# Kernel tuning notes

Measured on AMD Instinct MI355X. Metric: run time of the kernel, lower is better.

## Reference

```python
import jax, jax.numpy as jnp
import numpy as np

D_MODEL = 2048
N_HEADS = 16
HEAD_DIM = D_MODEL // N_HEADS  # 128
B, T = 2, 2048


def setup_inputs() -> dict:
    key = jax.random.key(0)
    ks = jax.random.split(key, 9)
    s = 0.02
    x = jax.random.normal(ks[0], (B, T, D_MODEL), dtype=jnp.float32)
    # Per-head projection weights (stacked over heads); torch Linear y = x @ W^T + b,
    # here W is stored as [H, d_model, head_dim] so y = einsum('btc,hcd->bhtd').
    Wq = jax.random.normal(ks[1], (N_HEADS, D_MODEL, HEAD_DIM), dtype=jnp.float32) * s
    bq = jax.random.normal(ks[2], (N_HEADS, HEAD_DIM), dtype=jnp.float32) * s
    Wk = jax.random.normal(ks[3], (N_HEADS, D_MODEL, HEAD_DIM), dtype=jnp.float32) * s
    bk = jax.random.normal(ks[4], (N_HEADS, HEAD_DIM), dtype=jnp.float32) * s
    Wv = jax.random.normal(ks[5], (N_HEADS, D_MODEL, HEAD_DIM), dtype=jnp.float32) * s
    bv = jax.random.normal(ks[6], (N_HEADS, HEAD_DIM), dtype=jnp.float32) * s
    Wo = jax.random.normal(ks[7], (D_MODEL, D_MODEL), dtype=jnp.float32) * s  # used as y @ Wo
    bo = jax.random.normal(ks[8], (D_MODEL,), dtype=jnp.float32) * s
    return {"x": x, "Wq": Wq, "bq": bq, "Wk": Wk, "bk": bk,
            "Wv": Wv, "bv": bv, "Wo": Wo, "bo": bo}


def reference(x, Wq, bq, Wk, bk, Wv, bv, Wo, bo):
    # x: [B, T, C]; per-head Q/K/V projections -> [B, H, T, D]
    Bn, Tn, C = x.shape
    H, _, D = Wq.shape
    scale = D ** (-0.5)
    q = jnp.einsum('btc,hcd->bhtd', x, Wq) + bq[None, :, None, :]
    k = jnp.einsum('btc,hcd->bhtd', x, Wk) + bk[None, :, None, :]
    v = jnp.einsum('btc,hcd->bhtd', x, Wv) + bv[None, :, None, :]
    # scores [B, H, T, T] with additive causal mask (finfo.min above the diagonal)
    scores = jnp.einsum('bhtd,bhsd->bhts', q, k) * scale
    neg = jnp.finfo(scores.dtype).min
    causal = jnp.triu(jnp.full((Tn, Tn), neg, dtype=scores.dtype), k=1)
    probs = jax.nn.softmax(scores + causal, axis=-1)
    y = jnp.einsum('bhts,bhsd->bhtd', probs, v)  # [B, H, T, D]
    # concat heads along feature dim (head order preserved) then output projection
    y = y.transpose(0, 2, 1, 3).reshape(Bn, Tn, H * D)
    return y @ Wo + bo
```

## Files before the change

kernel.cpp:

```cpp
#include <hip/hip_runtime.h>
#include <stdint.h>

typedef unsigned short u16;
typedef __attribute__((ext_vector_type(4))) u16 u16x4;
typedef __attribute__((ext_vector_type(8))) u16 u16x8;
typedef __attribute__((ext_vector_type(8))) __bf16 bf16x8;
typedef __attribute__((ext_vector_type(4))) float f32x4;

#define D_MODEL 2048
#define N_HEADS 16
#define HEAD_DIM 128
#define BATCH 2
#define SEQ 2048
#define M_TOT (BATCH*SEQ)
#define N_QKV (3*D_MODEL)

__device__ __forceinline__ u16 f2b(float f) {
  union { float f; uint32_t u; } c; c.f = f;
  uint32_t u = c.u;
  uint32_t r = (u + 0x7fffu + ((u >> 16) & 1u)) >> 16;
  return (u16)r;
}

__device__ __forceinline__ void gl_lds16(const u16* g, u16* l) {
  __builtin_amdgcn_global_load_lds(
      (const __attribute__((address_space(1))) uint32_t*)g,
      (__attribute__((address_space(3))) uint32_t*)l, 16, 0, 0);
}


__global__ void cast_x_kernel(const float* __restrict__ x, u16* __restrict__ xb, int n) {
  int i = (blockIdx.x * blockDim.x + threadIdx.x) * 4;
  if (i >= n) return;
  f32x4 v = *(const f32x4*)(x + i);
  u16x4 o;
  o[0] = f2b(v[0]); o[1] = f2b(v[1]); o[2] = f2b(v[2]); o[3] = f2b(v[3]);
  *(u16x4*)(xb + i) = o;
}

__global__ void trans_wqkv_kernel(const float* __restrict__ Wq, const float* __restrict__ Wk,
                                  const float* __restrict__ Wv, u16* __restrict__ Wt) {
  __shared__ u16 Tl[128][72];
  const int hh = blockIdx.y;
  const int qkv = hh >> 4, h = hh & 15;
  const float* src = (qkv == 0 ? Wq : qkv == 1 ? Wk : Wv) + (size_t)h * 2048 * 128;
  const int k0 = blockIdx.x * 64;
  const int tid = threadIdx.x;
  for (int it = 0; it < 32; ++it) {
    int idx = it * 256 + tid;
    int k = idx >> 7, d = idx & 127;
    Tl[d][k] = f2b(src[(size_t)(k0 + k) * 128 + d]);
  }
  __syncthreads();
  for (int it = 0; it < 32; ++it) {
    int idx = it * 256 + tid;
    int d = idx >> 6, kk = idx & 63;
    Wt[(size_t)(hh * 128 + d) * 2048 + k0 + kk] = Tl[d][kk];
  }
}

__global__ void trans_wo_kernel(const float* __restrict__ Wo, u16* __restrict__ Wot) {
  __shared__ u16 Tl[128][72];
  const int k0 = blockIdx.x * 64;
  const int n0 = blockIdx.y * 128;
  const int tid = threadIdx.x;
  for (int it = 0; it < 32; ++it) {
    int idx = it * 256 + tid;
    int k = idx >> 7, n = idx & 127;
    Tl[n][k] = f2b(Wo[(size_t)(k0 + k) * 2048 + n0 + n]);
  }
  __syncthreads();
  for (int it = 0; it < 32; ++it) {
    int idx = it * 256 + tid;
    int d = idx >> 6, kk = idx & 63;
    Wot[(size_t)(n0 + d) * 2048 + k0 + kk] = Tl[d][kk];
  }
}

__global__ void transpose_v_kernel(const u16* __restrict__ vb, u16* __restrict__ vt) {
  __shared__ u16 Tl[128 * 65];
  const int bh = blockIdx.y;
  const int t0 = blockIdx.x * 64;
  const int tid = threadIdx.x;
  const u16* src = vb + (size_t)bh * 2048 * 128;
  u16* dstp = vt + (size_t)bh * 128 * 2048;
#pragma unroll
  for (int c = 0; c < 4; ++c) {
    int ci = c * 256 + tid;
    int tr = ci >> 4, d0 = (ci & 15) * 8;
    u16x8 v = *(const u16x8*)(src + (size_t)(t0 + tr) * 128 + d0);
#pragma unroll
    for (int e = 0; e < 8; ++e) Tl[(d0 + e) * 65 + tr] = v[e];
  }
  __syncthreads();
#pragma unroll
  for (int it = 0; it < 32; ++it) {
    int idx = it * 256 + tid;
    int d = idx >> 6, tt = idx & 63;
    dstp[(size_t)d * 2048 + t0 + ((tt & 15) * 4 + (tt >> 4))] = Tl[d * 65 + tt];
  }
}

template <int EPI>
__global__ __launch_bounds__(256) void gemm_kernel(
    const u16* __restrict__ A, const u16* __restrict__ B,
    u16* __restrict__ qo, u16* __restrict__ ko, u16* __restrict__ vo,
    const float* __restrict__ bq, const float* __restrict__ bk, const float* __restrict__ bv,
    float* __restrict__ outf, const float* __restrict__ bo) {
  __shared__ u16 As[128 * 32];
  __shared__ u16 Bs[128 * 32];
  constexpr int NX = (EPI == 0) ? 48 : 16;
  const int nwg = gridDim.x;
  const int q8 = nwg >> 3;
  const int bid0 = blockIdx.x;
  const int gid = (bid0 & 7) * q8 + (bid0 >> 3);
  const int m0 = (gid / NX) * 128, n0 = (gid % NX) * 128;

  const int tid = threadIdx.x;
  const int lane = tid & 63, wv = tid >> 6;
  const int wm = (wv >> 1) * 64, wn = (wv & 1) * 64;
  const int lr = lane & 15, lk = (lane >> 4) * 8;

  f32x4 zero = {0.f, 0.f, 0.f, 0.f};
  f32x4 acc[4][4];
#pragma unroll
  for (int i = 0; i < 4; ++i)
#pragma unroll
    for (int j = 0; j < 4; ++j) acc[i][j] = zero;

  const int e0 = tid * 8;
  const int row0 = e0 >> 5;
  const int col0 = e0 & 31;
  const u16* Ag = A + (size_t)(m0 + row0) * 2048 + col0;
  const u16* Bg = B + (size_t)(n0 + row0) * 2048 + col0;

  for (int kt = 0; kt < 2048; kt += 32) {
    gl_lds16(Ag + kt, As + e0);
    gl_lds16(Ag + kt + (size_t)64 * 2048, As + e0 + 64 * 32);
    gl_lds16(Bg + kt, Bs + e0);
    gl_lds16(Bg + kt + (size_t)64 * 2048, Bs + e0 + 64 * 32);
    __syncthreads();
    bf16x8 af[4], bfm[4];
#pragma unroll
    for (int i = 0; i < 4; ++i) af[i] = *(const bf16x8*)(As + (wm + i * 16 + lr) * 32 + lk);
#pragma unroll
    for (int j = 0; j < 4; ++j) bfm[j] = *(const bf16x8*)(Bs + (wn + j * 16 + lr) * 32 + lk);
#pragma unroll
    for (int i = 0; i < 4; ++i)
#pragma unroll
      for (int j = 0; j < 4; ++j)
        acc[i][j] = __builtin_amdgcn_mfma_f32_16x16x32_bf16(af[i], bfm[j], acc[i][j], 0, 0, 0);
    __syncthreads();
  }

  const int rbase = (lane >> 4) * 4;
  if (EPI == 0) {
    const int qkv = n0 >> 11, h = (n0 >> 7) & 15;
    const float* bias = (qkv == 0) ? bq : (qkv == 1) ? bk : bv;
    u16* dst = (qkv == 0) ? qo : (qkv == 1) ? ko : vo;
    const float qscale = 0.08838834764831845f * 1.4426950408889634f;
#pragma unroll
    for (int i = 0; i < 4; ++i)
#pragma unroll
      for (int j = 0; j < 4; ++j)
#pragma unroll
        for (int r = 0; r < 4; ++r) {
          int gm = m0 + wm + i * 16 + rbase + r;
          int d = wn + j * 16 + (lane & 15);
          float val = acc[i][j][r] + bias[h * 128 + d];
          if (qkv == 0) val *= qscale;
          int b = gm >> 11, t = gm & 2047;
          dst[((size_t)(b * 16 + h) * 2048 + t) * 128 + d] = f2b(val);
        }
  } else {
#pragma unroll
    for (int i = 0; i < 4; ++i)
#pragma unroll
      for (int j = 0; j < 4; ++j)
#pragma unroll
        for (int r = 0; r < 4; ++r) {
          int gm = m0 + wm + i * 16 + rbase + r;
          int gn = n0 + wn + j * 16 + (lane & 15);
          outf[(size_t)gm * 2048 + gn] = acc[i][j][r] + bo[gn];
        }
  }
}

__global__ __launch_bounds__(256) void attn_kernel(
    const u16* __restrict__ qg, const u16* __restrict__ kg,
    const u16* __restrict__ vtg, u16* __restrict__ y) {
  __shared__ u16 Kb[2][64 * 128];
  __shared__ u16 Vb[2][128 * 64];
  __shared__ u16 Pl[4][32 * 64];
  const int tid = threadIdx.x, lane = tid & 63, w = tid >> 6;
  const int bid = blockIdx.x;
  const int bh = bid & 31, qt = 15 - (bid >> 5);
  const int b = bh >> 4, h = bh & 15;
  const int lr = lane & 15, lk = (lane >> 4) * 8;
  const u16* Qp = qg + (size_t)bh * (2048 * 128);
  const u16* Kp = kg + (size_t)bh * (2048 * 128);
  const u16* Vp = vtg + (size_t)bh * (128 * 2048);

  int koff[4], voff[4], dstc[4];
#pragma unroll
  for (int c = 0; c < 4; ++c) {
    int ci = c * 256 + tid;
    dstc[c] = ci * 8;
    int kr = ci >> 4, kj = ci & 15;
    koff[c] = kr * 128 + (kj ^ (kr & 7)) * 8;
    int vd = ci >> 3, vj = ci & 7;
    voff[c] = vd * 2048 + (vj ^ (vd & 7)) * 8;
  }
  const int kxor = (lr & 7) << 4;
  const int rbase = (lane >> 4) * 4;
  const f32x4 zero = {0.f, 0.f, 0.f, 0.f};

  const int q0 = qt * 128;
  const int qw = q0 + w * 32;
  const int nt = 2 * qt + 2;

  bf16x8 qf[2][4];
#pragma unroll
  for (int s = 0; s < 2; ++s)
#pragma unroll
    for (int i = 0; i < 4; ++i)
      qf[s][i] = *(const bf16x8*)(Qp + (size_t)(qw + s * 16 + lr) * 128 + i * 32 + lk);

  f32x4 o[2][8];
#pragma unroll
  for (int s = 0; s < 2; ++s)
#pragma unroll
    for (int f = 0; f < 8; ++f) o[s][f] = zero;
  float mrow[2][4], lrow[2][4];
#pragma unroll
  for (int s = 0; s < 2; ++s)
#pragma unroll
    for (int r = 0; r < 4; ++r) { mrow[s][r] = -1e30f; lrow[s][r] = 0.f; }

#pragma unroll
  for (int c = 0; c < 4; ++c) gl_lds16(Kp + koff[c], Kb[0] + dstc[c]);
#pragma unroll
  for (int c = 0; c < 4; ++c) gl_lds16(Vp + voff[c], Vb[0] + dstc[c]);
  __syncthreads();

  int cur = 0;
  for (int t = 0; t < nt; ++t) {
    const int s0 = t * 64;
    if (t + 1 < nt) {
      const size_t skn = (size_t)(s0 + 64) * 128;
#pragma unroll
      for (int c = 0; c < 4; ++c) gl_lds16(Kp + skn + koff[c], Kb[cur ^ 1] + dstc[c]);
#pragma unroll
      for (int c = 0; c < 4; ++c) gl_lds16(Vp + (s0 + 64) + voff[c], Vb[cur ^ 1] + dstc[c]);
    }
    if (s0 <= qw + 31) {
      const char* Kc = (const char*)Kb[cur];
      f32x4 sf[2][4];
      __builtin_amdgcn_s_setprio(1);
#pragma unroll
      for (int sj = 0; sj < 4; ++sj) {
        f32x4 a0 = zero, a1 = zero;
#pragma unroll
        for (int i = 0; i < 4; ++i) {
          bf16x8 kf = *(const bf16x8*)(Kc + ((((sj * 16 + lr) * 256) + (i * 32 + lk) * 2) ^ kxor));
          a0 = __builtin_amdgcn_mfma_f32_16x16x32_bf16(qf[0][i], kf, a0, 0, 0, 0);
          a1 = __builtin_amdgcn_mfma_f32_16x16x32_bf16(qf[1][i], kf, a1, 0, 0, 0);
        }
        sf[0][sj] = a0; sf[1][sj] = a1;
      }
      __builtin_amdgcn_s_setprio(0);

      char* Pc = (char*)Pl[w];
      const bool diag = (s0 + 63 > qw);
      float pmax[2][4];
      bool need = false;
#pragma unroll
      for (int s = 0; s < 2; ++s)
#pragma unroll
        for (int r = 0; r < 4; ++r) {
          if (diag) {
            const int rq = qw + s * 16 + rbase + r;
#pragma unroll
            for (int sj = 0; sj < 4; ++sj)
              if (s0 + sj * 16 + lr > rq) sf[s][sj][r] = -1e30f;
          }
          float pm = fmaxf(fmaxf(sf[s][0][r], sf[s][1][r]),
                           fmaxf(sf[s][2][r], sf[s][3][r]));
          pmax[s][r] = pm;
          need |= (pm > mrow[s][r] + 8.f);
        }
      if (__any(need)) {
#pragma unroll
        for (int s = 0; s < 2; ++s)
#pragma unroll
          for (int r = 0; r < 4; ++r) {
            float pm = pmax[s][r];
            pm = fmaxf(pm, __shfl_xor(pm, 1));
            pm = fmaxf(pm, __shfl_xor(pm, 2));
            pm = fmaxf(pm, __shfl_xor(pm, 4));
            pm = fmaxf(pm, __shfl_xor(pm, 8));
            float mnew = fmaxf(mrow[s][r], pm);
            float sfac = __builtin_amdgcn_exp2f(mrow[s][r] - mnew);
            mrow[s][r] = mnew;
            lrow[s][r] *= sfac;
#pragma unroll
            for (int f = 0; f < 8; ++f) o[s][f][r] *= sfac;
          }
      }
#pragma unroll
      for (int s = 0; s < 2; ++s)
#pragma unroll
        for (int r = 0; r < 4; ++r) {
          const int prow = s * 16 + rbase + r;
          u16x4 pk;
          float ps = 0.f;
#pragma unroll
          for (int sj = 0; sj < 4; ++sj) {
            float p = __builtin_amdgcn_exp2f(sf[s][sj][r] - mrow[s][r]);
            ps += p;
            pk[sj] = f2b(p);
          }
          lrow[s][r] += ps;
          *(u16x4*)(Pc + ((prow * 128 + lr * 8) ^ ((prow & 7) << 4))) = pk;
        }

      const char* Vc = (const char*)Vb[cur];
      __builtin_amdgcn_s_setprio(1);
#pragma unroll
      for (int st = 0; st < 2; ++st) {
        bf16x8 pf0 = *(const bf16x8*)(Pc + (((lr * 128) + (st * 32 + lk) * 2) ^ kxor));
        bf16x8 pf1 = *(const bf16x8*)(Pc + ((((16 + lr) * 128) + (st * 32 + lk) * 2) ^ kxor));
#pragma unroll
        for (int f = 0; f < 8; ++f) {
          bf16x8 vf = *(const bf16x8*)(Vc + ((((f * 16 + lr) * 128) + (st * 32 + lk) * 2) ^ kxor));
          o[0][f] = __builtin_amdgcn_mfma_f32_16x16x32_bf16(pf0, vf, o[0][f], 0, 0, 0);
          o[1][f] = __builtin_amdgcn_mfma_f32_16x16x32_bf16(pf1, vf, o[1][f], 0, 0, 0);
        }
      }
      __builtin_amdgcn_s_setprio(0);
    }
    __syncthreads();
    cur ^= 1;
  }

#pragma unroll
  for (int s = 0; s < 2; ++s)
#pragma unroll
    for (int r = 0; r < 4; ++r) {
      float l = lrow[s][r];
      l += __shfl_xor(l, 1);
      l += __shfl_xor(l, 2);
      l += __shfl_xor(l, 4);
      l += __shfl_xor(l, 8);
      const float rinv = __builtin_amdgcn_rcpf(l);
      const int row = qw + s * 16 + rbase + r;
#pragma unroll
      for (int f = 0; f < 8; ++f)
        y[((size_t)b * 2048 + row) * 2048 + h * 128 + f * 16 + lr] =
            f2b(o[s][f][r] * rinv);
    }
}


extern "C" void kernel_launch(void* const* d_in, const int* in_sizes, int n_in,
                              void* d_out, int out_size, void* d_ws, size_t ws_size,
                              hipStream_t stream) {
  const float* x  = (const float*)d_in[0];
  const float* Wq = (const float*)d_in[1];
  const float* bq = (const float*)d_in[2];
  const float* Wk = (const float*)d_in[3];
  const float* bk = (const float*)d_in[4];
  const float* Wv = (const float*)d_in[5];
  const float* bv = (const float*)d_in[6];
  const float* Wo = (const float*)d_in[7];
  const float* bo = (const float*)d_in[8];
  float* out = (float*)d_out;
  char* ws = (char*)d_ws;

  u16* xb  = (u16*)(ws + 0);
  u16* Wt  = (u16*)(ws + 16777216);
  u16* qb  = (u16*)(ws + 41943040);
  u16* kb  = (u16*)(ws + 58720256);
  u16* vb  = (u16*)(ws + 75497472);
  u16* Wot = Wt;
  u16* vtb = (u16*)(ws + 25165824);
  u16* yb  = xb;

  cast_x_kernel<<<8192, 256, 0, stream>>>(x, xb, M_TOT * D_MODEL);
  trans_wqkv_kernel<<<dim3(32, 48), 256, 0, stream>>>(Wq, Wk, Wv, Wt);
  gemm_kernel<0><<<N_QKV / 128 * (M_TOT / 128), 256, 0, stream>>>(
      xb, Wt, qb, kb, vb, bq, bk, bv, nullptr, nullptr);
  trans_wo_kernel<<<dim3(32, 16), 256, 0, stream>>>(Wo, Wot);
  transpose_v_kernel<<<dim3(32, 32), 256, 0, stream>>>(vb, vtb);
  attn_kernel<<<512, 256, 0, stream>>>(qb, kb, vtb, yb);
  gemm_kernel<1><<<D_MODEL / 128 * (M_TOT / 128), 256, 0, stream>>>(
      yb, Wot, nullptr, nullptr, nullptr, nullptr, nullptr, nullptr, out, bo);
}
```

Baseline: 306.5 us.

## Rewrite GEMMs as 256x128 tiles with triple-buffered swizzled LDS pipeline

```diff
diff --git a/kernel.cpp b/kernel.cpp
--- a/kernel.cpp
+++ b/kernel.cpp
@@ -102,55 +102,119 @@
 }
 
 template <int EPI>
-__global__ __launch_bounds__(256) void gemm_kernel(
+__global__ __launch_bounds__(512, 2) void gemm256_kernel(
     const u16* __restrict__ A, const u16* __restrict__ B,
     u16* __restrict__ qo, u16* __restrict__ ko, u16* __restrict__ vo,
     const float* __restrict__ bq, const float* __restrict__ bk, const float* __restrict__ bv,
     float* __restrict__ outf, const float* __restrict__ bo) {
-  __shared__ u16 As[128 * 32];
-  __shared__ u16 Bs[128 * 32];
+  __shared__ u16 As[3][256 * 64];
+  __shared__ u16 Bs[3][128 * 64];
   constexpr int NX = (EPI == 0) ? 48 : 16;
-  const int nwg = gridDim.x;
-  const int q8 = nwg >> 3;
-  const int bid0 = blockIdx.x;
+  const int nwg = gridDim.x, q8 = nwg >> 3, bid0 = blockIdx.x;
   const int gid = (bid0 & 7) * q8 + (bid0 >> 3);
-  const int m0 = (gid / NX) * 128, n0 = (gid % NX) * 128;
+  const int m0 = (gid / NX) * 256, n0 = (gid % NX) * 128;
 
   const int tid = threadIdx.x;
-  const int lane = tid & 63, wv = tid >> 6;
-  const int wm = (wv >> 1) * 64, wn = (wv & 1) * 64;
+  const int lane = tid & 63, w = tid >> 6;
+  const int wm = (w >> 2) * 128, wn = (w & 3) * 32;
   const int lr = lane & 15, lk = (lane >> 4) * 8;
 
-  f32x4 zero = {0.f, 0.f, 0.f, 0.f};
-  f32x4 acc[4][4];
-#pragma unroll
-  for (int i = 0; i < 4; ++i)
-#pragma unroll
-    for (int j = 0; j < 4; ++j) acc[i][j] = zero;
-
-  const int e0 = tid * 8;
-  const int row0 = e0 >> 5;
-  const int col0 = e0 & 31;
-  const u16* Ag = A + (size_t)(m0 + row0) * 2048 + col0;
-  const u16* Bg = B + (size_t)(n0 + row0) * 2048 + col0;
-
-  for (int kt = 0; kt < 2048; kt += 32) {
-    gl_lds16(Ag + kt, As + e0);
-    gl_lds16(Ag + kt + (size_t)64 * 2048, As + e0 + 64 * 32);
-    gl_lds16(Bg + kt, Bs + e0);
-    gl_lds16(Bg + kt + (size_t)64 * 2048, Bs + e0 + 64 * 32);
-    __syncthreads();
-    bf16x8 af[4], bfm[4];
-#pragma unroll
-    for (int i = 0; i < 4; ++i) af[i] = *(const bf16x8*)(As + (wm + i * 16 + lr) * 32 + lk);
-#pragma unroll
-    for (int j = 0; j < 4; ++j) bfm[j] = *(const bf16x8*)(Bs + (wn + j * 16 + lr) * 32 + lk);
+  int aoff[4], adst[4], boff[2], bdst[2];
+#pragma unroll
+  for (int l = 0; l < 4; ++l) {
+    int ci = l * 512 + tid, row = ci >> 3, j = ci & 7;
+    aoff[l] = (m0 + row) * 2048 + (j ^ (row & 7)) * 8;
+    adst[l] = ci * 8;
+  }
+#pragma unroll
+  for (int l = 0; l < 2; ++l) {
+    int ci = l * 512 + tid, row = ci >> 3, j = ci & 7;
+    boff[l] = (n0 + row) * 2048 + (j ^ (row & 7)) * 8;
+    bdst[l] = ci * 8;
+  }
+
+  f32x4 acc[8][2];
+  const f32x4 zero = {0.f, 0.f, 0.f, 0.f};
+#pragma unroll
+  for (int i = 0; i < 8; ++i) { acc[i][0] = zero; acc[i][1] = zero; }
+
+#pragma unroll
+  for (int s = 0; s < 2; ++s) {
+#pragma unroll
+    for (int l = 0; l < 4; ++l) gl_lds16(A + aoff[l] + s * 64, As[s] + adst[l]);
+#pragma unroll
+    for (int l = 0; l < 2; ++l) gl_lds16(B + boff[l] + s * 64, Bs[s] + bdst[l]);
+  }
+  asm volatile("s_waitcnt vmcnt(6)" ::: "memory");
+  __builtin_amdgcn_s_barrier();
+
+  int slot = 0;
+  for (int kt = 0; kt < 32; ++kt) {
+    const char* Ac = (const char*)As[slot];
+    const char* Bc = (const char*)Bs[slot];
+    const int s2 = (slot + 2 >= 3) ? slot - 1 : slot + 2;
+    const bool st = (kt < 30);
+    const int k2 = (kt + 2) * 64;
+
+    bf16x8 af[4][2], bfr[2][2];
+#pragma unroll
+    for (int i = 0; i < 4; ++i) {
+      const int row = wm + i * 16 + lr;
+      const int rb = row * 128, rx = (row & 7) << 4;
+#pragma unroll
+      for (int kk = 0; kk < 2; ++kk)
+        af[i][kk] = *(const bf16x8*)(Ac + ((rb + (kk * 32 + lk) * 2) ^ rx));
+    }
+#pragma unroll
+    for (int j = 0; j < 2; ++j) {
+      const int row = wn + j * 16 + lr;
+      const int rb = row * 128, rx = (row & 7) << 4;
+#pragma unroll
+      for (int kk = 0; kk < 2; ++kk)
+        bfr[j][kk] = *(const bf16x8*)(Bc + ((rb + (kk * 32 + lk) * 2) ^ rx));
+    }
+    if (st) {
+      gl_lds16(A + aoff[0] + k2, As[s2] + adst[0]);
+      gl_lds16(A + aoff[1] + k2, As[s2] + adst[1]);
+      gl_lds16(B + boff[0] + k2, Bs[s2] + bdst[0]);
+    }
+    __builtin_amdgcn_s_setprio(1);
 #pragma unroll
     for (int i = 0; i < 4; ++i)
 #pragma unroll
-      for (int j = 0; j < 4; ++j)
-        acc[i][j] = __builtin_amdgcn_mfma_f32_16x16x32_bf16(af[i], bfm[j], acc[i][j], 0, 0, 0);
-    __syncthreads();
+      for (int j = 0; j < 2; ++j)
+#pragma unroll
+        for (int kk = 0; kk < 2; ++kk)
+          acc[i][j] = __builtin_amdgcn_mfma_f32_16x16x32_bf16(af[i][kk], bfr[j][kk], acc[i][j], 0, 0, 0);
+    __builtin_amdgcn_s_setprio(0);
+    __builtin_amdgcn_s_barrier();
+
+#pragma unroll
+    for (int i = 0; i < 4; ++i) {
+      const int row = wm + 64 + i * 16 + lr;
+      const int rb = row * 128, rx = (row & 7) << 4;
+#pragma unroll
+      for (int kk = 0; kk < 2; ++kk)
+        af[i][kk] = *(const bf16x8*)(Ac + ((rb + (kk * 32 + lk) * 2) ^ rx));
+    }
+    if (st) {
+      gl_lds16(A + aoff[2] + k2, As[s2] + adst[2]);
+      gl_lds16(A + aoff[3] + k2, As[s2] + adst[3]);
+      gl_lds16(B + boff[1] + k2, Bs[s2] + bdst[1]);
+    }
+    __builtin_amdgcn_s_setprio(1);
+#pragma unroll
+    for (int i = 0; i < 4; ++i)
+#pragma unroll
+      for (int j = 0; j < 2; ++j)
+#pragma unroll
+        for (int kk = 0; kk < 2; ++kk)
+          acc[i + 4][j] = __builtin_amdgcn_mfma_f32_16x16x32_bf16(af[i][kk], bfr[j][kk], acc[i + 4][j], 0, 0, 0);
+    __builtin_amdgcn_s_setprio(0);
+    if (kt == 30)      asm volatile("s_waitcnt vmcnt(0)" ::: "memory");
+    else if (kt < 30)  asm volatile("s_waitcnt vmcnt(6)" ::: "memory");
+    __builtin_amdgcn_s_barrier();
+    slot = (slot + 1 >= 3) ? 0 : slot + 1;
   }
 
   const int rbase = (lane >> 4) * 4;
@@ -160,13 +224,13 @@
     u16* dst = (qkv == 0) ? qo : (qkv == 1) ? ko : vo;
     const float qscale = 0.08838834764831845f * 1.4426950408889634f;
 #pragma unroll
-    for (int i = 0; i < 4; ++i)
-#pragma unroll
-      for (int j = 0; j < 4; ++j)
+    for (int i = 0; i < 8; ++i)
+#pragma unroll
+      for (int j = 0; j < 2; ++j)
 #pragma unroll
         for (int r = 0; r < 4; ++r) {
           int gm = m0 + wm + i * 16 + rbase + r;
-          int d = wn + j * 16 + (lane & 15);
+          int d = wn + j * 16 + lr;
           float val = acc[i][j][r] + bias[h * 128 + d];
           if (qkv == 0) val *= qscale;
           int b = gm >> 11, t = gm & 2047;
@@ -174,13 +238,13 @@
         }
   } else {
 #pragma unroll
-    for (int i = 0; i < 4; ++i)
-#pragma unroll
-      for (int j = 0; j < 4; ++j)
+    for (int i = 0; i < 8; ++i)
+#pragma unroll
+      for (int j = 0; j < 2; ++j)
 #pragma unroll
         for (int r = 0; r < 4; ++r) {
           int gm = m0 + wm + i * 16 + rbase + r;
-          int gn = n0 + wn + j * 16 + (lane & 15);
+          int gn = n0 + wn + j * 16 + lr;
           outf[(size_t)gm * 2048 + gn] = acc[i][j][r] + bo[gn];
         }
   }
@@ -388,11 +452,11 @@
 
   cast_x_kernel<<<8192, 256, 0, stream>>>(x, xb, M_TOT * D_MODEL);
   trans_wqkv_kernel<<<dim3(32, 48), 256, 0, stream>>>(Wq, Wk, Wv, Wt);
-  gemm_kernel<0><<<N_QKV / 128 * (M_TOT / 128), 256, 0, stream>>>(
+  gemm256_kernel<0><<<768, 512, 0, stream>>>(
       xb, Wt, qb, kb, vb, bq, bk, bv, nullptr, nullptr);
   trans_wo_kernel<<<dim3(32, 16), 256, 0, stream>>>(Wo, Wot);
   transpose_v_kernel<<<dim3(32, 32), 256, 0, stream>>>(vb, vtb);
   attn_kernel<<<512, 256, 0, stream>>>(qb, kb, vtb, yb);
-  gemm_kernel<1><<<D_MODEL / 128 * (M_TOT / 128), 256, 0, stream>>>(
+  gemm256_kernel<1><<<256, 512, 0, stream>>>(
       yb, Wot, nullptr, nullptr, nullptr, nullptr, nullptr, nullptr, out, bo);
 }
```

Result: faster. 287.8 us (-6.1%).

## Rewrite GEMMs with 256-wide tiles, 4-stage LDS pipeline and swizzled layout

Applied to the files above, without the earlier changes.

```diff
diff --git a/kernel.cpp b/kernel.cpp
--- a/kernel.cpp
+++ b/kernel.cpp
@@ -26,6 +26,14 @@
   __builtin_amdgcn_global_load_lds(
       (const __attribute__((address_space(1))) uint32_t*)g,
       (__attribute__((address_space(3))) uint32_t*)l, 16, 0, 0);
+}
+
+template <int N> __device__ __forceinline__ void waitvm() {
+  if constexpr (N == 8)      asm volatile("s_waitcnt vmcnt(8)" ::: "memory");
+  else if constexpr (N == 6) asm volatile("s_waitcnt vmcnt(6)" ::: "memory");
+  else if constexpr (N == 4) asm volatile("s_waitcnt vmcnt(4)" ::: "memory");
+  else if constexpr (N == 3) asm volatile("s_waitcnt vmcnt(3)" ::: "memory");
+  else                       asm volatile("s_waitcnt vmcnt(0)" ::: "memory");
 }
 
 
@@ -101,86 +109,135 @@
   }
 }
 
-template <int EPI>
-__global__ __launch_bounds__(256) void gemm_kernel(
+template <int EPI, int BM>
+__global__ __launch_bounds__(512, 2) void gemm256_kernel(
     const u16* __restrict__ A, const u16* __restrict__ B,
     u16* __restrict__ qo, u16* __restrict__ ko, u16* __restrict__ vo,
     const float* __restrict__ bq, const float* __restrict__ bk, const float* __restrict__ bv,
     float* __restrict__ outf, const float* __restrict__ bo) {
-  __shared__ u16 As[128 * 32];
-  __shared__ u16 Bs[128 * 32];
-  constexpr int NX = (EPI == 0) ? 48 : 16;
-  const int nwg = gridDim.x;
-  const int q8 = nwg >> 3;
-  const int bid0 = blockIdx.x;
+  constexpr int IM  = BM / 32;
+  constexpr int LPA = BM / 128;
+  constexpr int LP  = LPA + 2;
+  constexpr int ASZ = BM * 32;
+  constexpr int BSZ = 256 * 32;
+  __shared__ u16 HA[4 * ASZ];
+  __shared__ u16 HB[4 * BSZ];
+
+  constexpr int NX = (EPI == 0) ? 24 : 8;
+  const int nwg = gridDim.x, q8 = nwg >> 3, bid0 = blockIdx.x;
   const int gid = (bid0 & 7) * q8 + (bid0 >> 3);
-  const int m0 = (gid / NX) * 128, n0 = (gid % NX) * 128;
+  const int m0 = (gid / NX) * BM, n0 = (gid % NX) * 256;
 
   const int tid = threadIdx.x;
-  const int lane = tid & 63, wv = tid >> 6;
-  const int wm = (wv >> 1) * 64, wn = (wv & 1) * 64;
-  const int lr = lane & 15, lk = (lane >> 4) * 8;
-
-  f32x4 zero = {0.f, 0.f, 0.f, 0.f};
-  f32x4 acc[4][4];
-#pragma unroll
-  for (int i = 0; i < 4; ++i)
+  const int lane = tid & 63, w = tid >> 6;
+  const int wm = (w >> 2) * (BM / 2), wn = (w & 3) * 64;
+  const int lr = lane & 15;
+  const int ck = (lane >> 4) * 16;
+
+  int aoff[LPA], adst[LPA], boff[2], bdst[2];
+#pragma unroll
+  for (int l = 0; l < LPA; ++l) {
+    int ci = l * 512 + tid, row = ci >> 2, j = ci & 3;
+    aoff[l] = (m0 + row) * 2048 + (j ^ ((row >> 1) & 3)) * 8;
+    adst[l] = ci * 8;
+  }
+#pragma unroll
+  for (int l = 0; l < 2; ++l) {
+    int ci = l * 512 + tid, row = ci >> 2, j = ci & 3;
+    boff[l] = (n0 + row) * 2048 + (j ^ ((row >> 1) & 3)) * 8;
+    bdst[l] = ci * 8;
+  }
+
+  f32x4 acc[IM][4];
+  const f32x4 zero = {0.f, 0.f, 0.f, 0.f};
+#pragma unroll
+  for (int i = 0; i < IM; ++i)
 #pragma unroll
     for (int j = 0; j < 4; ++j) acc[i][j] = zero;
 
-  const int e0 = tid * 8;
-  const int row0 = e0 >> 5;
-  const int col0 = e0 & 31;
-  const u16* Ag = A + (size_t)(m0 + row0) * 2048 + col0;
-  const u16* Bg = B + (size_t)(n0 + row0) * 2048 + col0;
-
-  for (int kt = 0; kt < 2048; kt += 32) {
-    gl_lds16(Ag + kt, As + e0);
-    gl_lds16(Ag + kt + (size_t)64 * 2048, As + e0 + 64 * 32);
-    gl_lds16(Bg + kt, Bs + e0);
-    gl_lds16(Bg + kt + (size_t)64 * 2048, Bs + e0 + 64 * 32);
-    __syncthreads();
-    bf16x8 af[4], bfm[4];
-#pragma unroll
-    for (int i = 0; i < 4; ++i) af[i] = *(const bf16x8*)(As + (wm + i * 16 + lr) * 32 + lk);
-#pragma unroll
-    for (int j = 0; j < 4; ++j) bfm[j] = *(const bf16x8*)(Bs + (wn + j * 16 + lr) * 32 + lk);
-#pragma unroll
-    for (int i = 0; i < 4; ++i)
-#pragma unroll
-      for (int j = 0; j < 4; ++j)
-        acc[i][j] = __builtin_amdgcn_mfma_f32_16x16x32_bf16(af[i], bfm[j], acc[i][j], 0, 0, 0);
-    __syncthreads();
-  }
+#pragma unroll
+  for (int s = 0; s < 3; ++s) {
+#pragma unroll
+    for (int l = 0; l < LPA; ++l) gl_lds16(A + aoff[l] + s * 32, HA + s * ASZ + adst[l]);
+#pragma unroll
+    for (int l = 0; l < 2; ++l)   gl_lds16(B + boff[l] + s * 32, HB + s * BSZ + bdst[l]);
+  }
+  waitvm<2 * LP>();
+  __builtin_amdgcn_s_barrier();
+
+#define GPHASE(S, S3, DOSTAGE, H)                                                         \
+  {                                                                                       \
+    if (DOSTAGE) {                                                                        \
+      const int k2 = (H + 3) * 32;                                                        \
+      _Pragma("unroll")                                                                   \
+      for (int l = 0; l < LPA; ++l) gl_lds16(A + aoff[l] + k2, HA + (S3) * ASZ + adst[l]);\
+      _Pragma("unroll")                                                                   \
+      for (int l = 0; l < 2; ++l)   gl_lds16(B + boff[l] + k2, HB + (S3) * BSZ + bdst[l]);\
+    }                                                                                     \
+    const char* Ac = (const char*)(HA + (S) * ASZ);                                       \
+    const char* Bc = (const char*)(HB + (S) * BSZ);                                       \
+    bf16x8 af[IM], bfr[4];                                                                \
+    _Pragma("unroll")                                                                     \
+    for (int i = 0; i < IM; ++i) {                                                        \
+      int r = wm + i * 16 + lr;                                                           \
+      af[i] = *(const bf16x8*)(Ac + r * 64 + (ck ^ (((r >> 1) & 3) << 4)));               \
+    }                                                                                     \
+    _Pragma("unroll")                                                                     \
+    for (int j = 0; j < 4; ++j) {                                                         \
+      int r = wn + j * 16 + lr;                                                           \
+      bfr[j] = *(const bf16x8*)(Bc + r * 64 + (ck ^ (((r >> 1) & 3) << 4)));              \
+    }                                                                                     \
+    __builtin_amdgcn_s_setprio(1);                                                        \
+    _Pragma("unroll")                                                                     \
+    for (int i = 0; i < IM; ++i)                                                          \
+      _Pragma("unroll")                                                                   \
+      for (int j = 0; j < 4; ++j)                                                         \
+        acc[i][j] = __builtin_amdgcn_mfma_f32_16x16x32_bf16(af[i], bfr[j], acc[i][j], 0, 0, 0); \
+    __builtin_amdgcn_s_setprio(0);                                                        \
+  }
+
+  for (int kt = 0; kt < 15; ++kt) {
+    const int h0 = kt * 4;
+    GPHASE(0, 3, true, h0 + 0); waitvm<2 * LP>(); __builtin_amdgcn_s_barrier();
+    GPHASE(1, 0, true, h0 + 1); waitvm<2 * LP>(); __builtin_amdgcn_s_barrier();
+    GPHASE(2, 1, true, h0 + 2); waitvm<2 * LP>(); __builtin_amdgcn_s_barrier();
+    GPHASE(3, 2, true, h0 + 3); waitvm<2 * LP>(); __builtin_amdgcn_s_barrier();
+  }
+  GPHASE(0, 3, true,  60); waitvm<2 * LP>(); __builtin_amdgcn_s_barrier();
+  GPHASE(1, 0, false, 61); waitvm<LP>();     __builtin_amdgcn_s_barrier();
+  GPHASE(2, 0, false, 62); waitvm<0>();      __builtin_amdgcn_s_barrier();
+  GPHASE(3, 0, false, 63);
+#undef GPHASE
 
   const int rbase = (lane >> 4) * 4;
   if (EPI == 0) {
-    const int qkv = n0 >> 11, h = (n0 >> 7) & 15;
+    const int qkv = n0 >> 11;
     const float* bias = (qkv == 0) ? bq : (qkv == 1) ? bk : bv;
     u16* dst = (qkv == 0) ? qo : (qkv == 1) ? ko : vo;
     const float qscale = 0.08838834764831845f * 1.4426950408889634f;
 #pragma unroll
-    for (int i = 0; i < 4; ++i)
+    for (int i = 0; i < IM; ++i)
 #pragma unroll
       for (int j = 0; j < 4; ++j)
 #pragma unroll
         for (int r = 0; r < 4; ++r) {
           int gm = m0 + wm + i * 16 + rbase + r;
-          int d = wn + j * 16 + (lane & 15);
-          float val = acc[i][j][r] + bias[h * 128 + d];
+          int n = n0 + wn + j * 16 + lr;
+          int h = (n >> 7) & 15, d = n & 127;
+          float val = acc[i][j][r] + bias[n & 2047];
           if (qkv == 0) val *= qscale;
           int b = gm >> 11, t = gm & 2047;
           dst[((size_t)(b * 16 + h) * 2048 + t) * 128 + d] = f2b(val);
         }
   } else {
 #pragma unroll
-    for (int i = 0; i < 4; ++i)
+    for (int i = 0; i < IM; ++i)
 #pragma unroll
       for (int j = 0; j < 4; ++j)
 #pragma unroll
         for (int r = 0; r < 4; ++r) {
           int gm = m0 + wm + i * 16 + rbase + r;
-          int gn = n0 + wn + j * 16 + (lane & 15);
+          int gn = n0 + wn + j * 16 + lr;
           outf[(size_t)gm * 2048 + gn] = acc[i][j][r] + bo[gn];
         }
   }
@@ -388,11 +445,11 @@
 
   cast_x_kernel<<<8192, 256, 0, stream>>>(x, xb, M_TOT * D_MODEL);
   trans_wqkv_kernel<<<dim3(32, 48), 256, 0, stream>>>(Wq, Wk, Wv, Wt);
-  gemm_kernel<0><<<N_QKV / 128 * (M_TOT / 128), 256, 0, stream>>>(
+  gemm256_kernel<0, 256><<<384, 512, 0, stream>>>(
       xb, Wt, qb, kb, vb, bq, bk, bv, nullptr, nullptr);
   trans_wo_kernel<<<dim3(32, 16), 256, 0, stream>>>(Wo, Wot);
   transpose_v_kernel<<<dim3(32, 32), 256, 0, stream>>>(vb, vtb);
   attn_kernel<<<512, 256, 0, stream>>>(qb, kb, vtb, yb);
-  gemm_kernel<1><<<D_MODEL / 128 * (M_TOT / 128), 256, 0, stream>>>(
+  gemm256_kernel<1, 128><<<256, 512, 0, stream>>>(
       yb, Wot, nullptr, nullptr, nullptr, nullptr, nullptr, nullptr, out, bo);
 }
```

New measurement: 310.2 us. No clear change (+1.2%).

## Rewrite GEMMs with 512-thread ping-pong pipeline, swizzled LDS and larger N tiles

Applied to the files above, without the earlier changes.

```diff
diff --git a/kernel.cpp b/kernel.cpp
--- a/kernel.cpp
+++ b/kernel.cpp
@@ -26,6 +26,14 @@
   __builtin_amdgcn_global_load_lds(
       (const __attribute__((address_space(1))) uint32_t*)g,
       (__attribute__((address_space(3))) uint32_t*)l, 16, 0, 0);
+}
+
+template <int N> __device__ __forceinline__ void waitvm() {
+  if constexpr (N == 5)      asm volatile("s_waitcnt vmcnt(5)" ::: "memory");
+  else if constexpr (N == 4) asm volatile("s_waitcnt vmcnt(4)" ::: "memory");
+  else if constexpr (N == 3) asm volatile("s_waitcnt vmcnt(3)" ::: "memory");
+  else if constexpr (N == 2) asm volatile("s_waitcnt vmcnt(2)" ::: "memory");
+  else                       asm volatile("s_waitcnt vmcnt(0)" ::: "memory");
 }
 
 
@@ -101,88 +109,188 @@
   }
 }
 
-template <int EPI>
-__global__ __launch_bounds__(256) void gemm_kernel(
+template <int EPI, int BN>
+__global__ __launch_bounds__(512, 2) void gemm4p_kernel(
     const u16* __restrict__ A, const u16* __restrict__ B,
     u16* __restrict__ qo, u16* __restrict__ ko, u16* __restrict__ vo,
     const float* __restrict__ bq, const float* __restrict__ bk, const float* __restrict__ bv,
     float* __restrict__ outf, const float* __restrict__ bo) {
-  __shared__ u16 As[128 * 32];
-  __shared__ u16 Bs[128 * 32];
-  constexpr int NX = (EPI == 0) ? 48 : 16;
-  const int nwg = gridDim.x;
-  const int q8 = nwg >> 3;
-  const int bid0 = blockIdx.x;
+  constexpr int BNW = BN / 4, SW = BNW / 2, NBF = SW / 16;
+  constexpr int NBQ = NBF;
+  constexpr int ASZ = 128 * 64, BSZ = BN * 64;
+  __shared__ u16 HA[2 * ASZ];
+  __shared__ u16 HB[2 * BSZ];
+  constexpr int NXT = (EPI == 0) ? (6144 / BN) : (2048 / BN);
+  const int nwg = gridDim.x, q8 = nwg >> 3, bid0 = blockIdx.x;
   const int gid = (bid0 & 7) * q8 + (bid0 >> 3);
-  const int m0 = (gid / NX) * 128, n0 = (gid % NX) * 128;
-
-  const int tid = threadIdx.x;
-  const int lane = tid & 63, wv = tid >> 6;
-  const int wm = (wv >> 1) * 64, wn = (wv & 1) * 64;
+  const int m0 = (gid / NXT) * 128, n0 = (gid % NXT) * BN;
+
+  const int tid = threadIdx.x, lane = tid & 63, w = tid >> 6;
+  const int wm = (w >> 2) * 64, wn = (w & 3) * BNW;
   const int lr = lane & 15, lk = (lane >> 4) * 8;
-
-  f32x4 zero = {0.f, 0.f, 0.f, 0.f};
-  f32x4 acc[4][4];
-#pragma unroll
-  for (int i = 0; i < 4; ++i)
-#pragma unroll
-    for (int j = 0; j < 4; ++j) acc[i][j] = zero;
-
-  const int e0 = tid * 8;
-  const int row0 = e0 >> 5;
-  const int col0 = e0 & 31;
-  const u16* Ag = A + (size_t)(m0 + row0) * 2048 + col0;
-  const u16* Bg = B + (size_t)(n0 + row0) * 2048 + col0;
-
-  for (int kt = 0; kt < 2048; kt += 32) {
-    gl_lds16(Ag + kt, As + e0);
-    gl_lds16(Ag + kt + (size_t)64 * 2048, As + e0 + 64 * 32);
-    gl_lds16(Bg + kt, Bs + e0);
-    gl_lds16(Bg + kt + (size_t)64 * 2048, Bs + e0 + 64 * 32);
-    __syncthreads();
-    bf16x8 af[4], bfm[4];
-#pragma unroll
-    for (int i = 0; i < 4; ++i) af[i] = *(const bf16x8*)(As + (wm + i * 16 + lr) * 32 + lk);
-#pragma unroll
-    for (int j = 0; j < 4; ++j) bfm[j] = *(const bf16x8*)(Bs + (wn + j * 16 + lr) * 32 + lk);
-#pragma unroll
-    for (int i = 0; i < 4; ++i)
-#pragma unroll
-      for (int j = 0; j < 4; ++j)
-        acc[i][j] = __builtin_amdgcn_mfma_f32_16x16x32_bf16(af[i], bfm[j], acc[i][j], 0, 0, 0);
-    __syncthreads();
-  }
+  const int kb0 = lk * 2;
+  const int rx = (lr & 7) << 4;
+  const int ws4 = (w & 3) * SW;
+
+  int aoff[2], boff[2][NBQ];
+#pragma unroll
+  for (int l = 0; l < 2; ++l) {
+    int ci = l * 512 + tid, row = ci >> 3, j = ci & 7;
+    aoff[l] = (m0 + row) * 2048 + (j ^ (row & 7)) * 8;
+  }
+#pragma unroll
+  for (int hb = 0; hb < 2; ++hb)
+#pragma unroll
+    for (int l = 0; l < NBQ; ++l) {
+      int cj = l * 512 + tid;
+      int s = cj / (SW * 8), rem = cj % (SW * 8);
+      int r = rem >> 3, j = rem & 7;
+      int row = s * BNW + hb * SW + r;
+      boff[hb][l] = (n0 + row) * 2048 + (j ^ (row & 7)) * 8;
+    }
+  const int dst0 = tid * 8;
+
+  f32x4 acc[2][2][2][NBF];
+  const f32x4 zero = {0.f, 0.f, 0.f, 0.f};
+#pragma unroll
+  for (int ah = 0; ah < 2; ++ah)
+#pragma unroll
+    for (int ai = 0; ai < 2; ++ai)
+#pragma unroll
+      for (int hb = 0; hb < 2; ++hb)
+#pragma unroll
+        for (int bj = 0; bj < NBF; ++bj) acc[ah][ai][hb][bj] = zero;
+
+  bf16x8 af[2][2][2], bfr[2][NBF][2];
+
+#define READ_A(AH, ACB)                                                              \
+  _Pragma("unroll") for (int ai = 0; ai < 2; ++ai) {                                 \
+    int row = wm + (AH) * 32 + ai * 16 + lr;                                         \
+    _Pragma("unroll") for (int kk = 0; kk < 2; ++kk)                                 \
+      af[AH][ai][kk] = *(const bf16x8*)((ACB) + row * 128 + ((kb0 + kk * 64) ^ rx)); \
+  }
+#define READ_B(HB, BCB)                                                              \
+  _Pragma("unroll") for (int bj = 0; bj < NBF; ++bj) {                               \
+    int row = ((HB) * 4) * SW + ws4 + bj * 16 + lr;                                  \
+    _Pragma("unroll") for (int kk = 0; kk < 2; ++kk)                                 \
+      bfr[HB][bj][kk] = *(const bf16x8*)((BCB) + row * 128 + ((kb0 + kk * 64) ^ rx));\
+  }
+#define MMA(AH, HB)                                                                  \
+  __builtin_amdgcn_s_setprio(1);                                                     \
+  _Pragma("unroll") for (int ai = 0; ai < 2; ++ai)                                   \
+    _Pragma("unroll") for (int bj = 0; bj < NBF; ++bj)                               \
+      _Pragma("unroll") for (int kk = 0; kk < 2; ++kk)                               \
+        acc[AH][ai][HB][bj] = __builtin_amdgcn_mfma_f32_16x16x32_bf16(               \
+            af[AH][ai][kk], bfr[HB][bj][kk], acc[AH][ai][HB][bj], 0, 0, 0);          \
+  __builtin_amdgcn_s_setprio(0);
+#define BAR __builtin_amdgcn_s_barrier()
+#define LGKM0 asm volatile("s_waitcnt lgkmcnt(0)" ::: "memory")
+
+#pragma unroll
+  for (int l = 0; l < 2; ++l) gl_lds16(A + aoff[l], HA + l * 4096 + dst0);
+#pragma unroll
+  for (int hb = 0; hb < 2; ++hb)
+#pragma unroll
+    for (int l = 0; l < NBQ; ++l)
+      gl_lds16(B + boff[hb][l], HB + hb * (BSZ / 2) + l * 4096 + dst0);
+  waitvm<0>();
+  BAR;
+
+  for (int kt = 0; kt < 31; ++kt) {
+    const int c = kt & 1, ns = c ^ 1;
+    const char* Acb = (const char*)(HA + c * ASZ);
+    const char* Bcb = (const char*)(HB + c * BSZ);
+    const int k2 = (kt + 1) * 64;
+    READ_A(0, Acb); READ_B(0, Bcb);
+#pragma unroll
+    for (int l = 0; l < 2; ++l) gl_lds16(A + aoff[l] + k2, HA + ns * ASZ + l * 4096 + dst0);
+#pragma unroll
+    for (int l = 0; l < NBQ; ++l)
+      gl_lds16(B + boff[0][l] + k2, HB + ns * BSZ + l * 4096 + dst0);
+    BAR; LGKM0;
+    MMA(0, 0);
+    waitvm<NBQ + 2>();
+    BAR;
+    READ_B(1, Bcb);
+#pragma unroll
+    for (int l = 0; l < NBQ; ++l)
+      gl_lds16(B + boff[1][l] + k2, HB + ns * BSZ + (BSZ / 2) + l * 4096 + dst0);
+    BAR; LGKM0;
+    MMA(0, 1);
+    BAR;
+    READ_A(1, Acb);
+    BAR; LGKM0;
+    MMA(1, 1);
+    BAR;
+    MMA(1, 0);
+    waitvm<NBQ>();
+    BAR;
+  }
+  {
+    const char* Acb = (const char*)(HA + ASZ);
+    const char* Bcb = (const char*)(HB + BSZ);
+    READ_A(0, Acb); READ_B(0, Bcb);
+    BAR; LGKM0;
+    MMA(0, 0);
+    waitvm<0>();
+    BAR;
+    READ_B(1, Bcb);
+    BAR; LGKM0;
+    MMA(0, 1);
+    BAR;
+    READ_A(1, Acb);
+    BAR; LGKM0;
+    MMA(1, 1);
+    MMA(1, 0);
+  }
+#undef READ_A
+#undef READ_B
+#undef MMA
+#undef BAR
+#undef LGKM0
 
   const int rbase = (lane >> 4) * 4;
   if (EPI == 0) {
-    const int qkv = n0 >> 11, h = (n0 >> 7) & 15;
-    const float* bias = (qkv == 0) ? bq : (qkv == 1) ? bk : bv;
-    u16* dst = (qkv == 0) ? qo : (qkv == 1) ? ko : vo;
     const float qscale = 0.08838834764831845f * 1.4426950408889634f;
 #pragma unroll
-    for (int i = 0; i < 4; ++i)
-#pragma unroll
-      for (int j = 0; j < 4; ++j)
-#pragma unroll
-        for (int r = 0; r < 4; ++r) {
-          int gm = m0 + wm + i * 16 + rbase + r;
-          int d = wn + j * 16 + (lane & 15);
-          float val = acc[i][j][r] + bias[h * 128 + d];
-          if (qkv == 0) val *= qscale;
-          int b = gm >> 11, t = gm & 2047;
-          dst[((size_t)(b * 16 + h) * 2048 + t) * 128 + d] = f2b(val);
-        }
+    for (int hb = 0; hb < 2; ++hb)
+#pragma unroll
+      for (int bj = 0; bj < NBF; ++bj) {
+        const int n = n0 + wn + hb * SW + bj * 16 + lr;
+        const int qkv = n >> 11, hh = (n >> 7) & 15, d = n & 127;
+        const float* bias = (qkv == 0) ? bq : (qkv == 1) ? bk : bv;
+        u16* dst = (qkv == 0) ? qo : (qkv == 1) ? ko : vo;
+        const float bv_ = bias[n & 2047];
+#pragma unroll
+        for (int ah = 0; ah < 2; ++ah)
+#pragma unroll
+          for (int ai = 0; ai < 2; ++ai)
+#pragma unroll
+            for (int r = 0; r < 4; ++r) {
+              int gm = m0 + wm + ah * 32 + ai * 16 + rbase + r;
+              float val = acc[ah][ai][hb][bj][r] + bv_;
+              if (qkv == 0) val *= qscale;
+              int b = gm >> 11, t = gm & 2047;
+              dst[((size_t)(b * 16 + hh) * 2048 + t) * 128 + d] = f2b(val);
+            }
+      }
   } else {
 #pragma unroll
-    for (int i = 0; i < 4; ++i)
-#pragma unroll
-      for (int j = 0; j < 4; ++j)
-#pragma unroll
-        for (int r = 0; r < 4; ++r) {
-          int gm = m0 + wm + i * 16 + rbase + r;
-          int gn = n0 + wn + j * 16 + (lane & 15);
-          outf[(size_t)gm * 2048 + gn] = acc[i][j][r] + bo[gn];
-        }
+    for (int hb = 0; hb < 2; ++hb)
+#pragma unroll
+      for (int bj = 0; bj < NBF; ++bj) {
+        const int gn = n0 + wn + hb * SW + bj * 16 + lr;
+        const float bv_ = bo[gn];
+#pragma unroll
+        for (int ah = 0; ah < 2; ++ah)
+#pragma unroll
+          for (int ai = 0; ai < 2; ++ai)
+#pragma unroll
+            for (int r = 0; r < 4; ++r) {
+              int gm = m0 + wm + ah * 32 + ai * 16 + rbase + r;
+              outf[(size_t)gm * 2048 + gn] = acc[ah][ai][hb][bj][r] + bv_;
+            }
+      }
   }
 }
 
@@ -388,11 +496,11 @@
 
   cast_x_kernel<<<8192, 256, 0, stream>>>(x, xb, M_TOT * D_MODEL);
   trans_wqkv_kernel<<<dim3(32, 48), 256, 0, stream>>>(Wq, Wk, Wv, Wt);
-  gemm_kernel<0><<<N_QKV / 128 * (M_TOT / 128), 256, 0, stream>>>(
+  gemm4p_kernel<0, 384><<<512, 512, 0, stream>>>(
       xb, Wt, qb, kb, vb, bq, bk, bv, nullptr, nullptr);
   trans_wo_kernel<<<dim3(32, 16), 256, 0, stream>>>(Wo, Wot);
   transpose_v_kernel<<<dim3(32, 32), 256, 0, stream>>>(vb, vtb);
   attn_kernel<<<512, 256, 0, stream>>>(qb, kb, vtb, yb);
-  gemm_kernel<1><<<D_MODEL / 128 * (M_TOT / 128), 256, 0, stream>>>(
+  gemm4p_kernel<1, 256><<<256, 512, 0, stream>>>(
       yb, Wot, nullptr, nullptr, nullptr, nullptr, nullptr, nullptr, out, bo);
 }
```

Measured after the change: 298.0 us. 2.8% less time.
